# Performance work log

Measured on AMD Instinct MI355X. Metric: run time of the kernel, lower is better.

Reference implementation:

```python
import jax, jax.numpy as jnp
import numpy as np

B, C, H, W = 16, 64, 256, 256


def setup_inputs() -> dict:
    key = jax.random.key(0)
    k1, k2, k3 = jax.random.split(key, 3)
    x = jax.random.normal(k1, (B, C, H, W), dtype=jnp.float32)
    # module init: xpos ~ U(-1e-8, 1e-8) (effectively 0), ypos ~ U(-3, 3)
    xpos = jax.random.normal(k2, (H,), dtype=jnp.float32) * 1e-8
    ypos = jnp.clip(jax.random.normal(k3, (H,), dtype=jnp.float32) * 2.0, -3.0, 3.0)
    return {"x": x, "xpos": xpos, "ypos": ypos, "stride": 1}


def reference(x, xpos, ypos, stride):
    # out[b,c,h,w] = x[b,c, clamp(h + int(ypos[h]*stride)), clamp(w + int(xpos[w]*stride))]
    Hh, Ww = x.shape[2], x.shape[3]
    # Python int() truncates toward zero -> jnp.trunc
    sh = jnp.clip(jnp.arange(Hh) + jnp.trunc(ypos * stride).astype(jnp.int32), 0, Hh - 1)
    sw = jnp.clip(jnp.arange(Ww) + jnp.trunc(xpos * stride).astype(jnp.int32), 0, Ww - 1)
    # gather along H then W via broadcasted advanced indexing
    return x[:, :, sh[:, None], sw[None, :]]
```

## Files before the change

kernel.cpp:

```cpp
#include <hip/hip_runtime.h>


constexpr int Bc = 16;
constexpr int Cc = 64;
constexpr int Hc = 256;
constexpr int Wc = 256;

__global__ __launch_bounds__(256) void shift_kernel(
    const float* __restrict__ x,
    const float* __restrict__ xpos,
    const float* __restrict__ ypos,
    const int* __restrict__ stride_p,
    float* __restrict__ out)
{
    const int stride = *stride_p;

    const long long tid = (long long)blockIdx.x * blockDim.x + threadIdx.x;
    const int lane_in_row = (int)(tid & (Wc / 4 - 1));
    const int w0 = lane_in_row * 4;
    const long long rowIdx = tid >> 6;
    const int h = (int)(rowIdx & (Hc - 1));

    int sh = h + (int)(ypos[h] * (float)stride);
    sh = min(max(sh, 0), Hc - 1);

    const long long planeIdx = rowIdx >> 8;
    const float* __restrict__ src = x + (planeIdx * Hc + sh) * (long long)Wc;

    float r[4];
#pragma unroll
    for (int i = 0; i < 4; ++i) {
        const int w = w0 + i;
        int sw = w + (int)(xpos[w] * (float)stride);
        sw = min(max(sw, 0), Wc - 1);
        r[i] = src[sw];
    }

    float4 v = make_float4(r[0], r[1], r[2], r[3]);
    *reinterpret_cast<float4*>(out + rowIdx * (long long)Wc + w0) = v;
}

extern "C" void kernel_launch(void* const* d_in, const int* in_sizes, int n_in,
                              void* d_out, int out_size, void* d_ws, size_t ws_size,
                              hipStream_t stream)
{
    const float* x     = (const float*)d_in[0];
    const float* xpos  = (const float*)d_in[1];
    const float* ypos  = (const float*)d_in[2];
    const int* stride  = (const int*)d_in[3];
    float* out         = (float*)d_out;

    const long long total_threads = (long long)Bc * Cc * Hc * (Wc / 4);
    const int block = 256;
    const long long grid = total_threads / block;

    shift_kernel<<<(int)grid, block, 0, stream>>>(x, xpos, ypos, stride, out);
}
```

Baseline: 444.6 us.

## Stage source rows in LDS with float4 loads, gather along W from shared memory

Each block now handles 16 output rows of one plane. It loads the shifted source rows with coalesced float4 reads into LDS, then each thread gathers its column shift from LDS and writes scalar, coalesced stores. This replaces the per-thread scalar gathered global loads and repeated xpos reads with vector global loads, at the cost of a block barrier, 16KB of LDS per block and scalar stores instead of float4 stores.

```diff
diff --git a/kernel.cpp b/kernel.cpp
--- a/kernel.cpp
+++ b/kernel.cpp
@@ -5,6 +5,7 @@
 constexpr int Cc = 64;
 constexpr int Hc = 256;
 constexpr int Wc = 256;
+constexpr int ROWS = 16;
 
 __global__ __launch_bounds__(256) void shift_kernel(
     const float* __restrict__ x,
@@ -13,46 +14,50 @@
     const int* __restrict__ stride_p,
     float* __restrict__ out)
 {
+    __shared__ float lds[ROWS][Wc];
+
     const int stride = *stride_p;
+    const int t  = threadIdx.x;
+    const int wv = t >> 6;
+    const int ln = t & 63;
 
-    const long long tid = (long long)blockIdx.x * blockDim.x + threadIdx.x;
-    const int lane_in_row = (int)(tid & (Wc / 4 - 1));
-    const int w0 = lane_in_row * 4;
-    const long long rowIdx = tid >> 6;
-    const int h = (int)(rowIdx & (Hc - 1));
+    const int plane = blockIdx.x >> 4;
+    const int h0    = (blockIdx.x & 15) * ROWS;
 
-    int sh = h + (int)(ypos[h] * (float)stride);
-    sh = min(max(sh, 0), Hc - 1);
+    const float* __restrict__ src_plane = x + (long long)plane * Hc * Wc;
 
-    const long long planeIdx = rowIdx >> 8;
-    const float* __restrict__ src = x + (planeIdx * Hc + sh) * (long long)Wc;
-
-    float r[4];
 #pragma unroll
-    for (int i = 0; i < 4; ++i) {
-        const int w = w0 + i;
-        int sw = w + (int)(xpos[w] * (float)stride);
-        sw = min(max(sw, 0), Wc - 1);
-        r[i] = src[sw];
+    for (int k = 0; k < 4; ++k) {
+        const int r = wv + 4 * k;
+        const int h = h0 + r;
+        int sh = h + (int)(ypos[h] * (float)stride);
+        sh = min(max(sh, 0), Hc - 1);
+        const float4 v = *reinterpret_cast<const float4*>(src_plane + sh * Wc + ln * 4);
+        *reinterpret_cast<float4*>(&lds[r][ln * 4]) = v;
     }
 
-    float4 v = make_float4(r[0], r[1], r[2], r[3]);
-    *reinterpret_cast<float4*>(out + rowIdx * (long long)Wc + w0) = v;
+    __syncthreads();
+
+    int sw = t + (int)(xpos[t] * (float)stride);
+    sw = min(max(sw, 0), Wc - 1);
+
+    float* __restrict__ dst = out + ((long long)plane * Hc + h0) * Wc + t;
+#pragma unroll
+    for (int r = 0; r < ROWS; ++r) {
+        dst[r * Wc] = lds[r][sw];
+    }
 }
 
 extern "C" void kernel_launch(void* const* d_in, const int* in_sizes, int n_in,
                               void* d_out, int out_size, void* d_ws, size_t ws_size,
                               hipStream_t stream)
 {
-    const float* x     = (const float*)d_in[0];
-    const float* xpos  = (const float*)d_in[1];
-    const float* ypos  = (const float*)d_in[2];
-    const int* stride  = (const int*)d_in[3];
-    float* out         = (float*)d_out;
+    const float* x    = (const float*)d_in[0];
+    const float* xpos = (const float*)d_in[1];
+    const float* ypos = (const float*)d_in[2];
+    const int* stride = (const int*)d_in[3];
+    float* out        = (float*)d_out;
 
-    const long long total_threads = (long long)Bc * Cc * Hc * (Wc / 4);
-    const int block = 256;
-    const long long grid = total_threads / block;
-
-    shift_kernel<<<(int)grid, block, 0, stream>>>(x, xpos, ypos, stride, out);
+    const int blocks = Bc * Cc * (Hc / ROWS);
+    shift_kernel<<<blocks, 256, 0, stream>>>(x, xpos, ypos, stride, out);
 }
```

Result: faster. 419.1 us (-5.7%).
